# Kernel optimization log

Measured on AMD Instinct MI355X. Metric: run time of the kernel, lower is better.

## Reference

```python
import jax, jax.numpy as jnp
import numpy as np

HEADS = 4
HID = 32
IN = 128
OUT = 8
N = 50000
E = 1600000


def setup_inputs() -> dict:
    key = jax.random.key(0)
    ks = jax.random.split(key, 12)
    x = jax.random.normal(ks[0], (N, IN), dtype=jnp.float32)
    edge_index = jax.random.randint(ks[1], (2, E), 0, N, dtype=jnp.int64)
    s = 0.05
    W1 = jax.random.normal(ks[2], (IN, HEADS * HID), dtype=jnp.float32) * s
    att_src1 = jax.random.normal(ks[3], (HEADS, HID), dtype=jnp.float32) * s
    att_dst1 = jax.random.normal(ks[4], (HEADS, HID), dtype=jnp.float32) * s
    b1 = jnp.zeros((HEADS * HID,), dtype=jnp.float32)
    W2 = jax.random.normal(ks[5], (HEADS * HID, HEADS * HID), dtype=jnp.float32) * s
    att_src2 = jax.random.normal(ks[6], (HEADS, HID), dtype=jnp.float32) * s
    att_dst2 = jax.random.normal(ks[7], (HEADS, HID), dtype=jnp.float32) * s
    b2 = jnp.zeros((HEADS * HID,), dtype=jnp.float32)
    Wout = jax.random.normal(ks[8], (HEADS * HID, OUT), dtype=jnp.float32) * s
    bout = jnp.zeros((OUT,), dtype=jnp.float32)
    return {"x": x, "edge_index": edge_index, "W1": W1, "att_src1": att_src1,
            "att_dst1": att_dst1, "b1": b1, "W2": W2, "att_src2": att_src2,
            "att_dst2": att_dst2, "b2": b2, "Wout": Wout, "bout": bout}


def gat_conv(x, src, dst, W, att_src, att_dst, b):
    n = x.shape[0]
    h = (x @ W).reshape(n, HEADS, HID)              # [N,H,C]
    a_s = (h * att_src).sum(-1)                      # [N,H]
    a_d = (h * att_dst).sum(-1)                      # [N,H]
    e = jax.nn.leaky_relu(a_s[src] + a_d[dst], 0.2)  # [E,H]
    # scatter-softmax over incoming edges of each destination node
    m = jax.ops.segment_max(e, dst, num_segments=n)
    e = jnp.exp(e - m[dst])
    denom = jax.ops.segment_sum(e, dst, num_segments=n)
    alpha = e / (denom[dst] + 1e-16)                 # [E,H]
    msg = h[src] * alpha[:, :, None]                 # [E,H,C]
    out = jax.ops.segment_sum(msg, dst, num_segments=n)
    return out.reshape(n, HEADS * HID) + b


def reference(x, edge_index, W1, att_src1, att_dst1, b1, W2, att_src2, att_dst2, b2, Wout, bout):
    n = x.shape[0]
    # GATConv adds self-loops by default
    loops = jnp.arange(n, dtype=edge_index.dtype)
    src = jnp.concatenate([edge_index[0], loops])
    dst = jnp.concatenate([edge_index[1], loops])
    # dropout p=0.6 is identity in eval mode
    h = gat_conv(x, src, dst, W1, att_src1, att_dst1, b1)
    h = jax.nn.elu(h)
    h = gat_conv(h, src, dst, W2, att_src2, att_dst2, b2)
    return h @ Wout + bout
```

## Files before the change

### kernel.cpp

```cpp
#include <hip/hip_runtime.h>
#include <hip/hip_fp16.h>
#include <math.h>

#define N_NODES 50000
#define E_EDGES 1600000
#define NE_TOT  (E_EDGES + N_NODES)

#define BSH 7
#define NBKT ((N_NODES + 127) >> 7)
#define EPW 4096
#define NWA ((NE_TOT + EPW - 1) / EPW)

#define CH 128


__device__ __forceinline__ void gemm_att_body(
    int bid, int t, float* Wl, float* xs,
    const float* __restrict__ X, const float* __restrict__ W,
    const float* __restrict__ attS, const float* __restrict__ attD,
    __half* __restrict__ H16, float* __restrict__ a_s, float* __restrict__ a_d) {
    int g = t >> 5, cl = t & 31, c4 = cl * 4;
    int rowbase = bid * 32;
    float4 acc[4];
    #pragma unroll
    for (int rr = 0; rr < 4; rr++) acc[rr] = make_float4(0.f, 0.f, 0.f, 0.f);

    for (int kp = 0; kp < 2; kp++) {
        __syncthreads();
        #pragma unroll
        for (int j = 0; j < 8; j++) {
            int f4 = t + 256 * j;
            int kk = f4 >> 5, cg = f4 & 31;
            *(float4*)&Wl[kk * 128 + cg * 4] =
                *(const float4*)&W[(kp * 64 + kk) * 128 + cg * 4];
        }
        #pragma unroll
        for (int j = 0; j < 2; j++) {
            int f4 = t + 256 * j;
            int r = f4 >> 4, k4 = f4 & 15;
            int grow = rowbase + r;
            float4 xv = make_float4(0.f, 0.f, 0.f, 0.f);
            if (grow < N_NODES) xv = *(const float4*)&X[grow * 128 + kp * 64 + k4 * 4];
            *(float4*)&xs[r * 64 + k4 * 4] = xv;
        }
        __syncthreads();
        #pragma unroll
        for (int k4 = 0; k4 < 16; k4++) {
            float4 xv[4];
            #pragma unroll
            for (int rr = 0; rr < 4; rr++)
                xv[rr] = *(float4*)&xs[(g * 4 + rr) * 64 + k4 * 4];
            #pragma unroll
            for (int kk = 0; kk < 4; kk++) {
                float4 wv = *(float4*)&Wl[(k4 * 4 + kk) * 128 + c4];
                #pragma unroll
                for (int rr = 0; rr < 4; rr++) {
                    float xc = (kk == 0) ? xv[rr].x : (kk == 1) ? xv[rr].y
                             : (kk == 2) ? xv[rr].z : xv[rr].w;
                    acc[rr].x += xc * wv.x;
                    acc[rr].y += xc * wv.y;
                    acc[rr].z += xc * wv.z;
                    acc[rr].w += xc * wv.w;
                }
            }
        }
    }

    float4 as4 = *(const float4*)&attS[c4];
    float4 ad4 = *(const float4*)&attD[c4];
    int head = cl >> 3;
    #pragma unroll
    for (int rr = 0; rr < 4; rr++) {
        int grow = rowbase + g * 4 + rr;
        float4 a = acc[rr];
        if (grow < N_NODES) {
            __half2 lo = __floats2half2_rn(a.x, a.y);
            __half2 hi = __floats2half2_rn(a.z, a.w);
            uint2 pk;
            pk.x = *(unsigned int*)&lo;
            pk.y = *(unsigned int*)&hi;
            *(uint2*)&H16[(size_t)grow * 128 + c4] = pk;
        }
        float ps = a.x * as4.x + a.y * as4.y + a.z * as4.z + a.w * as4.w;
        float pd = a.x * ad4.x + a.y * ad4.y + a.z * ad4.z + a.w * ad4.w;
        ps += __shfl_xor(ps, 1); ps += __shfl_xor(ps, 2); ps += __shfl_xor(ps, 4);
        pd += __shfl_xor(pd, 1); pd += __shfl_xor(pd, 2); pd += __shfl_xor(pd, 4);
        if ((cl & 7) == 0 && grow < N_NODES) {
            a_s[grow * 4 + head] = ps;
            a_d[grow * 4 + head] = pd;
        }
    }
}

__global__ __launch_bounds__(256) void k_hist_gemm(
    const int* __restrict__ ei, int* __restrict__ histG,
    const float* __restrict__ X, const float* __restrict__ W,
    const float* __restrict__ attS, const float* __restrict__ attD,
    __half* __restrict__ H16, float* __restrict__ a_s, float* __restrict__ a_d) {
    __shared__ __align__(16) char smem[40960];
    int t = threadIdx.x;
    if (blockIdx.x < NWA) {
        int* h = (int*)smem;
        for (int i = t; i < NBKT; i += 256) h[i] = 0;
        __syncthreads();
        int base = blockIdx.x * EPW;
        #pragma unroll 4
        for (int j = 0; j < EPW / 256; j++) {
            int e = base + t + 256 * j;
            if (e < NE_TOT) {
                int d = (e < E_EDGES) ? ei[E_EDGES + e] : (e - E_EDGES);
                atomicAdd(&h[d >> BSH], 1);
            }
        }
        __syncthreads();
        for (int i = t; i < NBKT; i += 256) histG[blockIdx.x * NBKT + i] = h[i];
    } else {
        float* Wl = (float*)smem;
        float* xs = (float*)(smem + 32768);
        gemm_att_body(blockIdx.x - NWA, t, Wl, xs, X, W, attS, attD, H16, a_s, a_d);
    }
}

__global__ __launch_bounds__(256) void k_gemm_att(
    const float* __restrict__ X, const float* __restrict__ W,
    const float* __restrict__ attS, const float* __restrict__ attD,
    __half* __restrict__ H16, float* __restrict__ a_s, float* __restrict__ a_d) {
    __shared__ float Wl[64 * 128];
    __shared__ float xs[32 * 64];
    gemm_att_body(blockIdx.x, threadIdx.x, Wl, xs, X, W, attS, attD, H16, a_s, a_d);
}


__global__ __launch_bounds__(512) void k_bktscan(int* __restrict__ histG,
                                                 int* __restrict__ bktTotal) {
    __shared__ int sh[512];
    int b = blockIdx.x;
    int t = threadIdx.x;
    int v = (t < NWA) ? histG[t * NBKT + b] : 0;
    sh[t] = v;
    __syncthreads();
    for (int d = 1; d < 512; d <<= 1) {
        int x = (t >= d) ? sh[t - d] : 0;
        __syncthreads();
        sh[t] += x;
        __syncthreads();
    }
    if (t < NWA) histG[t * NBKT + b] = sh[t] - v;
    if (t == 511) bktTotal[b] = sh[511];
}

__global__ __launch_bounds__(512) void k_bktbase(const int* __restrict__ bktTotal,
                                                 int* __restrict__ bktBase,
                                                 int* __restrict__ row_start) {
    __shared__ int sc[512];
    int t = threadIdx.x;
    int v = (t < NBKT) ? bktTotal[t] : 0;
    sc[t] = v;
    __syncthreads();
    for (int d = 1; d < 512; d <<= 1) {
        int x = (t >= d) ? sc[t - d] : 0;
        __syncthreads();
        sc[t] += x;
        __syncthreads();
    }
    if (t < NBKT) bktBase[t] = sc[t] - v;
    if (t == NBKT - 1) { bktBase[NBKT] = sc[t]; row_start[N_NODES] = sc[t]; }
}

__global__ __launch_bounds__(256) void k_binscatter(const int* __restrict__ ei,
                                                    const int* __restrict__ histG,
                                                    const int* __restrict__ bktBase,
                                                    unsigned int* __restrict__ pairs) {
    __shared__ int lofs[NBKT];
    int t = threadIdx.x;
    for (int i = t; i < NBKT; i += 256)
        lofs[i] = bktBase[i] + histG[blockIdx.x * NBKT + i];
    __syncthreads();
    int base = blockIdx.x * EPW;
    #pragma unroll 4
    for (int j = 0; j < EPW / 256; j++) {
        int e = base + t + 256 * j;
        if (e < NE_TOT) {
            int s, d;
            if (e < E_EDGES) { s = ei[e]; d = ei[E_EDGES + e]; }
            else             { s = d = e - E_EDGES; }
            int pos = atomicAdd(&lofs[d >> BSH], 1);
            pairs[pos] = ((unsigned int)d << 16) | (unsigned int)s;
        }
    }
}

__global__ __launch_bounds__(256) void k_bucketsort(const unsigned int* __restrict__ pairs,
                                                    const int* __restrict__ bktBase,
                                                    int* __restrict__ row_start,
                                                    unsigned short* __restrict__ col) {
    __shared__ int cnt[1 << BSH];
    __shared__ int sc[1 << BSH];
    __shared__ int cur[1 << BSH];
    int b = blockIdx.x, t = threadIdx.x;
    int nbeg = b << BSH;
    int ebeg = bktBase[b], eend = bktBase[b + 1];
    if (t < (1 << BSH)) cnt[t] = 0;
    __syncthreads();
    for (int j = ebeg + t; j < eend; j += 256)
        atomicAdd(&cnt[(int)(pairs[j] >> 16) - nbeg], 1);
    __syncthreads();
    int v = (t < (1 << BSH)) ? cnt[t] : 0;
    if (t < (1 << BSH)) sc[t] = v;
    __syncthreads();
    for (int d = 1; d < (1 << BSH); d <<= 1) {
        int x = 0;
        if (t < (1 << BSH) && t >= d) x = sc[t - d];
        __syncthreads();
        if (t < (1 << BSH)) sc[t] += x;
        __syncthreads();
    }
    if (t < (1 << BSH)) {
        int pos = ebeg + sc[t] - v;
        cur[t] = pos;
        int node = nbeg + t;
        if (node < N_NODES) row_start[node] = pos;
    }
    __syncthreads();
    for (int j = ebeg + t; j < eend; j += 256) {
        unsigned int p = pairs[j];
        int pos = atomicAdd(&cur[(int)(p >> 16) - nbeg], 1);
        col[pos] = (unsigned short)(p & 0xFFFFu);
    }
}


__device__ inline float sel4(float4 v, int i) {
    float r = v.x;
    if (i == 1) r = v.y;
    if (i == 2) r = v.z;
    if (i == 3) r = v.w;
    return r;
}

__device__ inline float4 expleaky4(float4 a, float4 b) {
    float4 e, p;
    e.x = a.x + b.x; e.x = e.x > 0.f ? e.x : 0.2f * e.x; p.x = __expf(e.x);
    e.y = a.y + b.y; e.y = e.y > 0.f ? e.y : 0.2f * e.y; p.y = __expf(e.y);
    e.z = a.z + b.z; e.z = e.z > 0.f ? e.z : 0.2f * e.z; p.z = __expf(e.z);
    e.w = a.w + b.w; e.w = e.w > 0.f ? e.w : 0.2f * e.w; p.w = __expf(e.w);
    return p;
}

#define ACC8(q, raw)                                              \
    do {                                                          \
        const __half2* hp_ = (const __half2*)&(raw);              \
        float2 f0_ = __half22float2(hp_[0]);                      \
        float2 f1_ = __half22float2(hp_[1]);                      \
        float2 f2_ = __half22float2(hp_[2]);                      \
        float2 f3_ = __half22float2(hp_[3]);                      \
        acc8[0] = fmaf((q), f0_.x, acc8[0]);                      \
        acc8[1] = fmaf((q), f0_.y, acc8[1]);                      \
        acc8[2] = fmaf((q), f1_.x, acc8[2]);                      \
        acc8[3] = fmaf((q), f1_.y, acc8[3]);                      \
        acc8[4] = fmaf((q), f2_.x, acc8[4]);                      \
        acc8[5] = fmaf((q), f2_.y, acc8[5]);                      \
        acc8[6] = fmaf((q), f3_.x, acc8[6]);                      \
        acc8[7] = fmaf((q), f3_.y, acc8[7]);                      \
    } while (0)

template<int MODE>
__global__ __launch_bounds__(256) void k_agg(
    const __half* __restrict__ H16, const float* __restrict__ a_s,
    const float* __restrict__ a_d, const int* __restrict__ row_start,
    const unsigned short* __restrict__ col, const float* __restrict__ bias,
    float* __restrict__ Hout,
    const float* __restrict__ Wout, const float* __restrict__ bout,
    float* __restrict__ out) {
    __shared__ float4 eS[4][CH];
    __shared__ int    sS[4][CH];
    __shared__ float  WoT[(MODE == 0) ? 1024 : 1];
    __shared__ float  boL[(MODE == 0) ? 8 : 1];

    if (MODE == 0) {
        for (int j = threadIdx.x; j < 1024; j += 256) {
            int o = j >> 7, k = j & 127;
            WoT[o * 128 + k] = Wout[k * 8 + o];
        }
        if (threadIdx.x < 8) boL[threadIdx.x] = bout[threadIdx.x];
        __syncthreads();
    }

    int wid = threadIdx.x >> 6;
    int lane = threadIdx.x & 63;
    int node = blockIdx.x * 4 + wid;
    if (node >= N_NODES) return;
    int beg = row_start[node], end = row_start[node + 1];
    int deg = end - beg;
    float4 ad4 = *(const float4*)&a_d[node * 4];
    float4* eA = eS[wid];
    int*    srcA = sS[wid];

    float4 s = make_float4(0.f, 0.f, 0.f, 0.f);
    for (int j = beg + lane; j < end; j += 64) {
        int src = (int)col[j];
        float4 av = *(const float4*)&a_s[src * 4];
        float4 p = expleaky4(av, ad4);
        int idx = j - beg;
        if (idx < CH) { srcA[idx] = src; eA[idx] = p; }
        s.x += p.x; s.y += p.y; s.z += p.z; s.w += p.w;
    }
    #pragma unroll
    for (int off = 32; off > 0; off >>= 1) {
        s.x += __shfl_xor(s.x, off);
        s.y += __shfl_xor(s.y, off);
        s.z += __shfl_xor(s.z, off);
        s.w += __shfl_xor(s.w, off);
    }
    float4 inv;
    inv.x = 1.f / (s.x + 1e-16f);
    inv.y = 1.f / (s.y + 1e-16f);
    inv.z = 1.f / (s.z + 1e-16f);
    inv.w = 1.f / (s.w + 1e-16f);

    int eslot = lane >> 4, cl16 = lane & 15, head = cl16 >> 2;
    const __half* hbase = H16 + cl16 * 8;
    const float* pA = (const float*)eA;
    float acc8[8];
    #pragma unroll
    for (int k = 0; k < 8; k++) acc8[k] = 0.f;

    int nst = min(deg, CH);
    int i = eslot;
    for (; i + 12 < nst; i += 16) {
        int s0 = srcA[i];
        int s1 = srcA[i + 4];
        int s2 = srcA[i + 8];
        int s3 = srcA[i + 12];
        float q0 = pA[i * 4 + head];
        float q1 = pA[(i + 4) * 4 + head];
        float q2 = pA[(i + 8) * 4 + head];
        float q3 = pA[(i + 12) * 4 + head];
        float4 r0 = *(const float4*)(hbase + (size_t)s0 * 128);
        float4 r1 = *(const float4*)(hbase + (size_t)s1 * 128);
        float4 r2 = *(const float4*)(hbase + (size_t)s2 * 128);
        float4 r3 = *(const float4*)(hbase + (size_t)s3 * 128);
        ACC8(q0, r0);
        ACC8(q1, r1);
        ACC8(q2, r2);
        ACC8(q3, r3);
    }
    for (; i < nst; i += 4) {
        int src = srcA[i];
        float p = pA[i * 4 + head];
        float4 raw = *(const float4*)(hbase + (size_t)src * 128);
        ACC8(p, raw);
    }
    for (int cb = beg + CH; cb < end; cb += CH) {
        int cnt = min(end - cb, CH);
        for (int idx = lane; idx < cnt; idx += 64) {
            int src = (int)col[cb + idx];
            float4 av = *(const float4*)&a_s[src * 4];
            float4 p = expleaky4(av, ad4);
            srcA[idx] = src; eA[idx] = p;
        }
        for (int ii = eslot; ii < cnt; ii += 4) {
            int src = srcA[ii];
            float p = pA[ii * 4 + head];
            float4 raw = *(const float4*)(hbase + (size_t)src * 128);
            ACC8(p, raw);
        }
    }

    #pragma unroll
    for (int k = 0; k < 8; k++) {
        acc8[k] += __shfl_xor(acc8[k], 16);
        acc8[k] += __shfl_xor(acc8[k], 32);
    }

    float ih = sel4(inv, head);
    if (MODE == 1) {
        if (eslot == 0) {
            const float* bp = &bias[cl16 * 8];
            float o[8];
            #pragma unroll
            for (int k = 0; k < 8; k++) {
                o[k] = acc8[k] * ih + bp[k];
                o[k] = o[k] > 0.f ? o[k] : expm1f(o[k]);
            }
            float* op = &Hout[(size_t)node * 128 + cl16 * 8];
            *(float4*)&op[0] = make_float4(o[0], o[1], o[2], o[3]);
            *(float4*)&op[4] = make_float4(o[4], o[5], o[6], o[7]);
        }
    } else {
        const float* bp = &bias[cl16 * 8];
        float4 oa, ob;
        oa.x = acc8[0] * ih + bp[0]; oa.y = acc8[1] * ih + bp[1];
        oa.z = acc8[2] * ih + bp[2]; oa.w = acc8[3] * ih + bp[3];
        ob.x = acc8[4] * ih + bp[4]; ob.y = acc8[5] * ih + bp[5];
        ob.z = acc8[6] * ih + bp[6]; ob.w = acc8[7] * ih + bp[7];
        int o0 = eslot * 2;
        float p0 = 0.f, p1 = 0.f;
        {
            float4 wa = *(float4*)&WoT[o0 * 128 + cl16 * 8];
            float4 wb = *(float4*)&WoT[o0 * 128 + cl16 * 8 + 4];
            p0 = oa.x * wa.x + oa.y * wa.y + oa.z * wa.z + oa.w * wa.w
               + ob.x * wb.x + ob.y * wb.y + ob.z * wb.z + ob.w * wb.w;
            float4 wc = *(float4*)&WoT[(o0 + 1) * 128 + cl16 * 8];
            float4 wd = *(float4*)&WoT[(o0 + 1) * 128 + cl16 * 8 + 4];
            p1 = oa.x * wc.x + oa.y * wc.y + oa.z * wc.z + oa.w * wc.w
               + ob.x * wd.x + ob.y * wd.y + ob.z * wd.z + ob.w * wd.w;
        }
        #pragma unroll
        for (int d = 1; d <= 8; d <<= 1) {
            p0 += __shfl_xor(p0, d);
            p1 += __shfl_xor(p1, d);
        }
        if (cl16 == 0) {
            float2 ov = make_float2(p0 + boL[o0], p1 + boL[o0 + 1]);
            *(float2*)&out[(size_t)node * 8 + o0] = ov;
        }
    }
}


extern "C" void kernel_launch(void* const* d_in, const int* in_sizes, int n_in,
                              void* d_out, int out_size, void* d_ws, size_t ws_size,
                              hipStream_t stream) {
    const float* x     = (const float*)d_in[0];
    const int*   ei    = (const int*)d_in[1];
    const float* W1    = (const float*)d_in[2];
    const float* attS1 = (const float*)d_in[3];
    const float* attD1 = (const float*)d_in[4];
    const float* b1    = (const float*)d_in[5];
    const float* W2    = (const float*)d_in[6];
    const float* attS2 = (const float*)d_in[7];
    const float* attD2 = (const float*)d_in[8];
    const float* b2    = (const float*)d_in[9];
    const float* Wout  = (const float*)d_in[10];
    const float* bout  = (const float*)d_in[11];
    float* out = (float*)d_out;

    char* ws = (char*)d_ws;
    size_t off = 0;
    auto alloc = [&](size_t bytes) -> void* {
        void* p = ws + off;
        off += (bytes + 255) & ~(size_t)255;
        return p;
    };
    float*          hB        = (float*)alloc((size_t)N_NODES * 128 * 4);
    __half*         h16       = (__half*)alloc((size_t)N_NODES * 128 * 2);
    float*          a_s       = (float*)alloc((size_t)N_NODES * 4 * 4);
    float*          a_d       = (float*)alloc((size_t)N_NODES * 4 * 4);
    int*            row_start = (int*)alloc((size_t)(N_NODES + 1) * 4);
    unsigned short* col       = (unsigned short*)alloc((size_t)NE_TOT * 2);
    int*            histG     = (int*)alloc((size_t)NWA * NBKT * 4);
    int*            bktTotal  = (int*)alloc((size_t)NBKT * 4);
    int*            bktBase   = (int*)alloc((size_t)(NBKT + 1) * 4);
    unsigned int*   pairs     = (unsigned int*)hB;

    int nbG = (N_NODES + 31) / 32;
    int nbA = (N_NODES + 3) / 4;

    k_hist_gemm<<<NWA + nbG, 256, 0, stream>>>(ei, histG, x, W1, attS1, attD1,
                                               h16, a_s, a_d);
    k_bktscan<<<NBKT, 512, 0, stream>>>(histG, bktTotal);
    k_bktbase<<<1, 512, 0, stream>>>(bktTotal, bktBase, row_start);
    k_binscatter<<<NWA, 256, 0, stream>>>(ei, histG, bktBase, pairs);
    k_bucketsort<<<NBKT, 256, 0, stream>>>(pairs, bktBase, row_start, col);

    k_agg<1><<<nbA, 256, 0, stream>>>(h16, a_s, a_d, row_start, col, b1, hB,
                                      Wout, bout, out);
    k_gemm_att<<<nbG, 256, 0, stream>>>(hB, W2, attS2, attD2, h16, a_s, a_d);
    k_agg<0><<<nbA, 256, 0, stream>>>(h16, a_s, a_d, row_start, col, b2, hB,
                                      Wout, bout, out);
}
```

Baseline: 255.0 us.

## Fuse CSR build kernels into one cooperative kernel with grid syncs

Merges the four CSR-construction kernels (bucket scan, base scan, bin scatter, bucket sort) into a single cooperative launch separated by grid-wide barriers. The scans now use 256 threads each handling two elements instead of 512 threads. The aim is to remove three kernel launch gaps and their inter-kernel drain and fill. In exchange, grid.sync has its own cost, the whole grid must be co-resident (403 blocks), and the single-block base scan leaves the other blocks idle at the barrier.

```diff
diff --git a/kernel.cpp b/kernel.cpp
--- a/kernel.cpp
+++ b/kernel.cpp
@@ -1,6 +1,9 @@
 #include <hip/hip_runtime.h>
 #include <hip/hip_fp16.h>
+#include <hip/hip_cooperative_groups.h>
 #include <math.h>
+
+namespace cg = cooperative_groups;
 
 #define N_NODES 50000
 #define E_EDGES 1600000
@@ -30,9 +33,9 @@
         #pragma unroll
         for (int j = 0; j < 8; j++) {
             int f4 = t + 256 * j;
-            int kk = f4 >> 5, cg = f4 & 31;
-            *(float4*)&Wl[kk * 128 + cg * 4] =
-                *(const float4*)&W[(kp * 64 + kk) * 128 + cg * 4];
+            int kk = f4 >> 5, cg2 = f4 & 31;
+            *(float4*)&Wl[kk * 128 + cg2 * 4] =
+                *(const float4*)&W[(kp * 64 + kk) * 128 + cg2 * 4];
         }
         #pragma unroll
         for (int j = 0; j < 2; j++) {
@@ -131,101 +134,111 @@
 }
 
 
-__global__ __launch_bounds__(512) void k_bktscan(int* __restrict__ histG,
-                                                 int* __restrict__ bktTotal) {
-    __shared__ int sh[512];
+__global__ __launch_bounds__(256) void k_csr(
+    const int* __restrict__ ei, int* __restrict__ histG,
+    int* __restrict__ bktTotal, int* __restrict__ bktBase,
+    int* __restrict__ row_start, unsigned int* __restrict__ pairs,
+    unsigned short* __restrict__ col) {
+    cg::grid_group grid = cg::this_grid();
+    __shared__ int smem[512];
+    int t = threadIdx.x;
     int b = blockIdx.x;
-    int t = threadIdx.x;
-    int v = (t < NWA) ? histG[t * NBKT + b] : 0;
-    sh[t] = v;
-    __syncthreads();
-    for (int d = 1; d < 512; d <<= 1) {
-        int x = (t >= d) ? sh[t - d] : 0;
-        __syncthreads();
-        sh[t] += x;
-        __syncthreads();
-    }
-    if (t < NWA) histG[t * NBKT + b] = sh[t] - v;
-    if (t == 511) bktTotal[b] = sh[511];
-}
-
-__global__ __launch_bounds__(512) void k_bktbase(const int* __restrict__ bktTotal,
-                                                 int* __restrict__ bktBase,
-                                                 int* __restrict__ row_start) {
-    __shared__ int sc[512];
-    int t = threadIdx.x;
-    int v = (t < NBKT) ? bktTotal[t] : 0;
-    sc[t] = v;
-    __syncthreads();
-    for (int d = 1; d < 512; d <<= 1) {
-        int x = (t >= d) ? sc[t - d] : 0;
-        __syncthreads();
-        sc[t] += x;
-        __syncthreads();
-    }
-    if (t < NBKT) bktBase[t] = sc[t] - v;
-    if (t == NBKT - 1) { bktBase[NBKT] = sc[t]; row_start[N_NODES] = sc[t]; }
-}
-
-__global__ __launch_bounds__(256) void k_binscatter(const int* __restrict__ ei,
-                                                    const int* __restrict__ histG,
-                                                    const int* __restrict__ bktBase,
-                                                    unsigned int* __restrict__ pairs) {
-    __shared__ int lofs[NBKT];
-    int t = threadIdx.x;
-    for (int i = t; i < NBKT; i += 256)
-        lofs[i] = bktBase[i] + histG[blockIdx.x * NBKT + i];
-    __syncthreads();
-    int base = blockIdx.x * EPW;
-    #pragma unroll 4
-    for (int j = 0; j < EPW / 256; j++) {
-        int e = base + t + 256 * j;
-        if (e < NE_TOT) {
-            int s, d;
-            if (e < E_EDGES) { s = ei[e]; d = ei[E_EDGES + e]; }
-            else             { s = d = e - E_EDGES; }
-            int pos = atomicAdd(&lofs[d >> BSH], 1);
-            pairs[pos] = ((unsigned int)d << 16) | (unsigned int)s;
-        }
-    }
-}
-
-__global__ __launch_bounds__(256) void k_bucketsort(const unsigned int* __restrict__ pairs,
-                                                    const int* __restrict__ bktBase,
-                                                    int* __restrict__ row_start,
-                                                    unsigned short* __restrict__ col) {
-    __shared__ int cnt[1 << BSH];
-    __shared__ int sc[1 << BSH];
-    __shared__ int cur[1 << BSH];
-    int b = blockIdx.x, t = threadIdx.x;
-    int nbeg = b << BSH;
-    int ebeg = bktBase[b], eend = bktBase[b + 1];
-    if (t < (1 << BSH)) cnt[t] = 0;
-    __syncthreads();
-    for (int j = ebeg + t; j < eend; j += 256)
-        atomicAdd(&cnt[(int)(pairs[j] >> 16) - nbeg], 1);
-    __syncthreads();
-    int v = (t < (1 << BSH)) ? cnt[t] : 0;
-    if (t < (1 << BSH)) sc[t] = v;
-    __syncthreads();
-    for (int d = 1; d < (1 << BSH); d <<= 1) {
-        int x = 0;
-        if (t < (1 << BSH) && t >= d) x = sc[t - d];
-        __syncthreads();
-        if (t < (1 << BSH)) sc[t] += x;
-        __syncthreads();
-    }
-    if (t < (1 << BSH)) {
-        int pos = ebeg + sc[t] - v;
-        cur[t] = pos;
-        int node = nbeg + t;
-        if (node < N_NODES) row_start[node] = pos;
-    }
-    __syncthreads();
-    for (int j = ebeg + t; j < eend; j += 256) {
-        unsigned int p = pairs[j];
-        int pos = atomicAdd(&cur[(int)(p >> 16) - nbeg], 1);
-        col[pos] = (unsigned short)(p & 0xFFFFu);
+
+    if (b < NBKT) {
+        int w0 = 2 * t, w1 = 2 * t + 1;
+        int a0 = (w0 < NWA) ? histG[w0 * NBKT + b] : 0;
+        int a1 = (w1 < NWA) ? histG[w1 * NBKT + b] : 0;
+        smem[w0] = a0; smem[w1] = a1;
+        __syncthreads();
+        for (int d = 1; d < 512; d <<= 1) {
+            int x0 = (w0 >= d) ? smem[w0 - d] : 0;
+            int x1 = (w1 >= d) ? smem[w1 - d] : 0;
+            __syncthreads();
+            smem[w0] += x0; smem[w1] += x1;
+            __syncthreads();
+        }
+        if (w0 < NWA) histG[w0 * NBKT + b] = smem[w0] - a0;
+        if (w1 < NWA) histG[w1 * NBKT + b] = smem[w1] - a1;
+        if (t == 255) bktTotal[b] = smem[511];
+    }
+    grid.sync();
+
+    if (b == 0) {
+        int i0 = 2 * t, i1 = 2 * t + 1;
+        int v0 = (i0 < NBKT) ? bktTotal[i0] : 0;
+        int v1 = (i1 < NBKT) ? bktTotal[i1] : 0;
+        smem[i0] = v0; smem[i1] = v1;
+        __syncthreads();
+        for (int d = 1; d < 512; d <<= 1) {
+            int x0 = (i0 >= d) ? smem[i0 - d] : 0;
+            int x1 = (i1 >= d) ? smem[i1 - d] : 0;
+            __syncthreads();
+            smem[i0] += x0; smem[i1] += x1;
+            __syncthreads();
+        }
+        if (i0 < NBKT) bktBase[i0] = smem[i0] - v0;
+        if (i1 < NBKT) bktBase[i1] = smem[i1] - v1;
+        if (t == 255) {
+            bktBase[NBKT] = smem[511];
+            row_start[N_NODES] = smem[511];
+        }
+    }
+    grid.sync();
+
+    {
+        int* lofs = smem;
+        for (int i = t; i < NBKT; i += 256)
+            lofs[i] = bktBase[i] + histG[b * NBKT + i];
+        __syncthreads();
+        int base = b * EPW;
+        #pragma unroll 4
+        for (int j = 0; j < EPW / 256; j++) {
+            int e = base + t + 256 * j;
+            if (e < NE_TOT) {
+                int s, d;
+                if (e < E_EDGES) { s = ei[e]; d = ei[E_EDGES + e]; }
+                else             { s = d = e - E_EDGES; }
+                int pos = atomicAdd(&lofs[d >> BSH], 1);
+                pairs[pos] = ((unsigned int)d << 16) | (unsigned int)s;
+            }
+        }
+        __syncthreads();
+    }
+    grid.sync();
+
+    if (b < NBKT) {
+        int* cnt = smem;
+        int* sc  = smem + 128;
+        int* cur = smem + 256;
+        int nbeg = b << BSH;
+        int ebeg = bktBase[b], eend = bktBase[b + 1];
+        if (t < (1 << BSH)) cnt[t] = 0;
+        __syncthreads();
+        for (int j = ebeg + t; j < eend; j += 256)
+            atomicAdd(&cnt[(int)(pairs[j] >> 16) - nbeg], 1);
+        __syncthreads();
+        int v = (t < (1 << BSH)) ? cnt[t] : 0;
+        if (t < (1 << BSH)) sc[t] = v;
+        __syncthreads();
+        for (int d = 1; d < (1 << BSH); d <<= 1) {
+            int x = 0;
+            if (t < (1 << BSH) && t >= d) x = sc[t - d];
+            __syncthreads();
+            if (t < (1 << BSH)) sc[t] += x;
+            __syncthreads();
+        }
+        if (t < (1 << BSH)) {
+            int pos = ebeg + sc[t] - v;
+            cur[t] = pos;
+            int node = nbeg + t;
+            if (node < N_NODES) row_start[node] = pos;
+        }
+        __syncthreads();
+        for (int j = ebeg + t; j < eend; j += 256) {
+            unsigned int p = pairs[j];
+            int pos = atomicAdd(&cur[(int)(p >> 16) - nbeg], 1);
+            col[pos] = (unsigned short)(p & 0xFFFFu);
+        }
     }
 }
 
@@ -459,10 +472,21 @@
 
     k_hist_gemm<<<NWA + nbG, 256, 0, stream>>>(ei, histG, x, W1, attS1, attD1,
                                                h16, a_s, a_d);
-    k_bktscan<<<NBKT, 512, 0, stream>>>(histG, bktTotal);
-    k_bktbase<<<1, 512, 0, stream>>>(bktTotal, bktBase, row_start);
-    k_binscatter<<<NWA, 256, 0, stream>>>(ei, histG, bktBase, pairs);
-    k_bucketsort<<<NBKT, 256, 0, stream>>>(pairs, bktBase, row_start, col);
+
+    {
+        const int* ei_a = ei;
+        int* histG_a = histG;
+        int* bktTotal_a = bktTotal;
+        int* bktBase_a = bktBase;
+        int* row_start_a = row_start;
+        unsigned int* pairs_a = pairs;
+        unsigned short* col_a = col;
+        void* args[] = { (void*)&ei_a, (void*)&histG_a, (void*)&bktTotal_a,
+                         (void*)&bktBase_a, (void*)&row_start_a,
+                         (void*)&pairs_a, (void*)&col_a };
+        hipLaunchCooperativeKernel((const void*)k_csr, dim3(NWA), dim3(256),
+                                   args, 0, stream);
+    }
 
     k_agg<1><<<nbA, 256, 0, stream>>>(h16, a_s, a_d, row_start, col, b1, hB,
                                       Wout, bout, out);
```

Measured after the change: 426.0 us. 1.67x slower.

## Replace multi-pass bucket prefix scan with fixed-capacity buckets and global atomic cursors

Applied to the files above, without the earlier changes.

Edge binning now happens in one kernel. Each work block reserves space in a fixed-capacity per-bucket region through global atomicAdd on a cursor, then scatters its edges directly. This removes the two scan kernels and the separate binscatter pass, and row extents become separate begin and end arrays. The cost is a memset, padded buckets, and a hard capacity limit (CAP 5120) that overflows if a bucket of 128 destination nodes receives more edges than that. It also makes the edge order within buckets nondeterministic.

```diff
diff --git a/kernel.cpp b/kernel.cpp
--- a/kernel.cpp
+++ b/kernel.cpp
@@ -10,7 +10,7 @@
 #define NBKT ((N_NODES + 127) >> 7)
 #define EPW 4096
 #define NWA ((NE_TOT + EPW - 1) / EPW)
-
+#define CAP 5120
 #define CH 128
 
 
@@ -30,9 +30,9 @@
         #pragma unroll
         for (int j = 0; j < 8; j++) {
             int f4 = t + 256 * j;
-            int kk = f4 >> 5, cg = f4 & 31;
-            *(float4*)&Wl[kk * 128 + cg * 4] =
-                *(const float4*)&W[(kp * 64 + kk) * 128 + cg * 4];
+            int kk = f4 >> 5, cg2 = f4 & 31;
+            *(float4*)&Wl[kk * 128 + cg2 * 4] =
+                *(const float4*)&W[(kp * 64 + kk) * 128 + cg2 * 4];
         }
         #pragma unroll
         for (int j = 0; j < 2; j++) {
@@ -92,15 +92,17 @@
     }
 }
 
-__global__ __launch_bounds__(256) void k_hist_gemm(
-    const int* __restrict__ ei, int* __restrict__ histG,
+__global__ __launch_bounds__(256) void k_hist_scatter_gemm(
+    const int* __restrict__ ei, int* __restrict__ cursor,
+    unsigned int* __restrict__ pairs,
     const float* __restrict__ X, const float* __restrict__ W,
     const float* __restrict__ attS, const float* __restrict__ attD,
     __half* __restrict__ H16, float* __restrict__ a_s, float* __restrict__ a_d) {
     __shared__ __align__(16) char smem[40960];
     int t = threadIdx.x;
     if (blockIdx.x < NWA) {
-        int* h = (int*)smem;
+        int* h    = (int*)smem;
+        int* wcur = ((int*)smem) + NBKT;
         for (int i = t; i < NBKT; i += 256) h[i] = 0;
         __syncthreads();
         int base = blockIdx.x * EPW;
@@ -113,7 +115,23 @@
             }
         }
         __syncthreads();
-        for (int i = t; i < NBKT; i += 256) histG[blockIdx.x * NBKT + i] = h[i];
+        for (int i = t; i < NBKT; i += 256) {
+            int c = h[i];
+            int rel = (c > 0) ? atomicAdd(&cursor[i], c) : 0;
+            wcur[i] = i * CAP + rel;
+        }
+        __syncthreads();
+        #pragma unroll 4
+        for (int j = 0; j < EPW / 256; j++) {
+            int e = base + t + 256 * j;
+            if (e < NE_TOT) {
+                int s, d;
+                if (e < E_EDGES) { s = ei[e]; d = ei[E_EDGES + e]; }
+                else             { s = d = e - E_EDGES; }
+                int pos = atomicAdd(&wcur[d >> BSH], 1);
+                pairs[pos] = ((unsigned int)d << 16) | (unsigned int)s;
+            }
+        }
     } else {
         float* Wl = (float*)smem;
         float* xs = (float*)(smem + 32768);
@@ -130,76 +148,17 @@
     gemm_att_body(blockIdx.x, threadIdx.x, Wl, xs, X, W, attS, attD, H16, a_s, a_d);
 }
 
-
-__global__ __launch_bounds__(512) void k_bktscan(int* __restrict__ histG,
-                                                 int* __restrict__ bktTotal) {
-    __shared__ int sh[512];
-    int b = blockIdx.x;
-    int t = threadIdx.x;
-    int v = (t < NWA) ? histG[t * NBKT + b] : 0;
-    sh[t] = v;
-    __syncthreads();
-    for (int d = 1; d < 512; d <<= 1) {
-        int x = (t >= d) ? sh[t - d] : 0;
-        __syncthreads();
-        sh[t] += x;
-        __syncthreads();
-    }
-    if (t < NWA) histG[t * NBKT + b] = sh[t] - v;
-    if (t == 511) bktTotal[b] = sh[511];
-}
-
-__global__ __launch_bounds__(512) void k_bktbase(const int* __restrict__ bktTotal,
-                                                 int* __restrict__ bktBase,
-                                                 int* __restrict__ row_start) {
-    __shared__ int sc[512];
-    int t = threadIdx.x;
-    int v = (t < NBKT) ? bktTotal[t] : 0;
-    sc[t] = v;
-    __syncthreads();
-    for (int d = 1; d < 512; d <<= 1) {
-        int x = (t >= d) ? sc[t - d] : 0;
-        __syncthreads();
-        sc[t] += x;
-        __syncthreads();
-    }
-    if (t < NBKT) bktBase[t] = sc[t] - v;
-    if (t == NBKT - 1) { bktBase[NBKT] = sc[t]; row_start[N_NODES] = sc[t]; }
-}
-
-__global__ __launch_bounds__(256) void k_binscatter(const int* __restrict__ ei,
-                                                    const int* __restrict__ histG,
-                                                    const int* __restrict__ bktBase,
-                                                    unsigned int* __restrict__ pairs) {
-    __shared__ int lofs[NBKT];
-    int t = threadIdx.x;
-    for (int i = t; i < NBKT; i += 256)
-        lofs[i] = bktBase[i] + histG[blockIdx.x * NBKT + i];
-    __syncthreads();
-    int base = blockIdx.x * EPW;
-    #pragma unroll 4
-    for (int j = 0; j < EPW / 256; j++) {
-        int e = base + t + 256 * j;
-        if (e < NE_TOT) {
-            int s, d;
-            if (e < E_EDGES) { s = ei[e]; d = ei[E_EDGES + e]; }
-            else             { s = d = e - E_EDGES; }
-            int pos = atomicAdd(&lofs[d >> BSH], 1);
-            pairs[pos] = ((unsigned int)d << 16) | (unsigned int)s;
-        }
-    }
-}
-
-__global__ __launch_bounds__(256) void k_bucketsort(const unsigned int* __restrict__ pairs,
-                                                    const int* __restrict__ bktBase,
-                                                    int* __restrict__ row_start,
-                                                    unsigned short* __restrict__ col) {
+__global__ __launch_bounds__(256) void k_bucketsort(
+    const unsigned int* __restrict__ pairs, const int* __restrict__ cursor,
+    int* __restrict__ rbeg, int* __restrict__ rend,
+    unsigned short* __restrict__ col) {
     __shared__ int cnt[1 << BSH];
     __shared__ int sc[1 << BSH];
     __shared__ int cur[1 << BSH];
     int b = blockIdx.x, t = threadIdx.x;
     int nbeg = b << BSH;
-    int ebeg = bktBase[b], eend = bktBase[b + 1];
+    int ebeg = b * CAP;
+    int eend = ebeg + cursor[b];
     if (t < (1 << BSH)) cnt[t] = 0;
     __syncthreads();
     for (int j = ebeg + t; j < eend; j += 256)
@@ -219,7 +178,7 @@
         int pos = ebeg + sc[t] - v;
         cur[t] = pos;
         int node = nbeg + t;
-        if (node < N_NODES) row_start[node] = pos;
+        if (node < N_NODES) { rbeg[node] = pos; rend[node] = pos + v; }
     }
     __syncthreads();
     for (int j = ebeg + t; j < eend; j += 256) {
@@ -267,7 +226,8 @@
 template<int MODE>
 __global__ __launch_bounds__(256) void k_agg(
     const __half* __restrict__ H16, const float* __restrict__ a_s,
-    const float* __restrict__ a_d, const int* __restrict__ row_start,
+    const float* __restrict__ a_d, const int* __restrict__ rbeg,
+    const int* __restrict__ rend,
     const unsigned short* __restrict__ col, const float* __restrict__ bias,
     float* __restrict__ Hout,
     const float* __restrict__ Wout, const float* __restrict__ bout,
@@ -290,7 +250,7 @@
     int lane = threadIdx.x & 63;
     int node = blockIdx.x * 4 + wid;
     if (node >= N_NODES) return;
-    int beg = row_start[node], end = row_start[node + 1];
+    int beg = rbeg[node], end = rend[node];
     int deg = end - beg;
     float4 ad4 = *(const float4*)&a_d[node * 4];
     float4* eA = eS[wid];
@@ -443,30 +403,27 @@
         off += (bytes + 255) & ~(size_t)255;
         return p;
     };
-    float*          hB        = (float*)alloc((size_t)N_NODES * 128 * 4);
-    __half*         h16       = (__half*)alloc((size_t)N_NODES * 128 * 2);
-    float*          a_s       = (float*)alloc((size_t)N_NODES * 4 * 4);
-    float*          a_d       = (float*)alloc((size_t)N_NODES * 4 * 4);
-    int*            row_start = (int*)alloc((size_t)(N_NODES + 1) * 4);
-    unsigned short* col       = (unsigned short*)alloc((size_t)NE_TOT * 2);
-    int*            histG     = (int*)alloc((size_t)NWA * NBKT * 4);
-    int*            bktTotal  = (int*)alloc((size_t)NBKT * 4);
-    int*            bktBase   = (int*)alloc((size_t)(NBKT + 1) * 4);
-    unsigned int*   pairs     = (unsigned int*)hB;
+    float*          hB     = (float*)alloc((size_t)N_NODES * 128 * 4);
+    __half*         h16    = (__half*)alloc((size_t)N_NODES * 128 * 2);
+    float*          a_s    = (float*)alloc((size_t)N_NODES * 4 * 4);
+    float*          a_d    = (float*)alloc((size_t)N_NODES * 4 * 4);
+    int*            rbeg   = (int*)alloc((size_t)N_NODES * 4);
+    int*            rend   = (int*)alloc((size_t)N_NODES * 4);
+    unsigned short* col    = (unsigned short*)alloc((size_t)NBKT * CAP * 2);
+    int*            cursor = (int*)alloc((size_t)NBKT * 4);
+    unsigned int*   pairs  = (unsigned int*)hB;
 
     int nbG = (N_NODES + 31) / 32;
     int nbA = (N_NODES + 3) / 4;
 
-    k_hist_gemm<<<NWA + nbG, 256, 0, stream>>>(ei, histG, x, W1, attS1, attD1,
-                                               h16, a_s, a_d);
-    k_bktscan<<<NBKT, 512, 0, stream>>>(histG, bktTotal);
-    k_bktbase<<<1, 512, 0, stream>>>(bktTotal, bktBase, row_start);
-    k_binscatter<<<NWA, 256, 0, stream>>>(ei, histG, bktBase, pairs);
-    k_bucketsort<<<NBKT, 256, 0, stream>>>(pairs, bktBase, row_start, col);
-
-    k_agg<1><<<nbA, 256, 0, stream>>>(h16, a_s, a_d, row_start, col, b1, hB,
+    hipMemsetAsync(cursor, 0, (size_t)NBKT * 4, stream);
+    k_hist_scatter_gemm<<<NWA + nbG, 256, 0, stream>>>(
+        ei, cursor, pairs, x, W1, attS1, attD1, h16, a_s, a_d);
+    k_bucketsort<<<NBKT, 256, 0, stream>>>(pairs, cursor, rbeg, rend, col);
+
+    k_agg<1><<<nbA, 256, 0, stream>>>(h16, a_s, a_d, rbeg, rend, col, b1, hB,
                                       Wout, bout, out);
     k_gemm_att<<<nbG, 256, 0, stream>>>(hB, W2, attS2, attD2, h16, a_s, a_d);
-    k_agg<0><<<nbA, 256, 0, stream>>>(h16, a_s, a_d, row_start, col, b2, hB,
+    k_agg<0><<<nbA, 256, 0, stream>>>(h16, a_s, a_d, rbeg, rend, col, b2, hB,
                                       Wout, bout, out);
 }
```

After: 253.9 us. About the same (-0.4%).
